# Kernel optimization log

Hardware: AMD Instinct MI355X
Metric: run time of the kernel (lower is better)

Reference implementation:

```python
import jax, jax.numpy as jnp
import numpy as np

H = 1024
W = 1024
SAMPLES_PER_SEG = 32
SIGMA_AA = 1.0
EDGE_CHUNK = 32  # matches torch chunk_size


def sample_bezier_path(control_points):
    # control_points: [N, 2], N = 3*S + 1 cubic segments
    N = control_points.shape[0]
    S = (N - 1) // 3
    idx = 3 * jnp.arange(S)
    p0 = control_points[idx][:, None, :]      # [S,1,2]
    p1 = control_points[idx + 1][:, None, :]
    p2 = control_points[idx + 2][:, None, :]
    p3 = control_points[idx + 3][:, None, :]
    t = jnp.linspace(0.0, 1.0, SAMPLES_PER_SEG, dtype=control_points.dtype)[None, :, None]  # [1,T,1]
    mt = 1.0 - t
    pts = (mt * mt * mt) * p0 + 3.0 * (mt * mt) * t * p1 + 3.0 * mt * (t * t) * p2 + (t * t * t) * p3
    return pts.reshape(S * SAMPLES_PER_SEG, 2)  # [M,2]


def compute_winding(path_points, sigma):
    # path_points: [M,2]; closed polygon edges (j -> (j+1)%M)
    M = path_points.shape[0]
    nxt = jnp.roll(path_points, -1, axis=0)
    x0, y0 = path_points[:, 0], path_points[:, 1]
    x1, y1 = nxt[:, 0], nxt[:, 1]
    dy = y1 - y0
    dx = x1 - x0
    # edges with |dy| < 1e-6 are skipped in the original (continue) -> zero contribution
    coeff = jnp.sign(dy) * (jnp.abs(dy) >= 1e-6).astype(path_points.dtype)
    grid_y = jnp.arange(H, dtype=path_points.dtype)  # rows
    grid_x = jnp.arange(W, dtype=path_points.dtype)  # cols

    n_chunks = M // EDGE_CHUNK
    def chunk_it(a):
        return a.reshape(n_chunks, EDGE_CHUNK)

    def body(acc, c):
        cx0, cy0, cdy, cdx, cc = c  # each [CH]
        t_cross = (grid_y[None, :] - cy0[:, None]) / (cdy[:, None] + 1e-8)          # [CH,H]
        x_cross = cx0[:, None] + t_cross * cdx[:, None]                              # [CH,H]
        valid_t = jax.nn.sigmoid(t_cross * 20.0) * jax.nn.sigmoid((1.0 - t_cross) * 20.0)  # [CH,H]
        crosses = jax.nn.sigmoid((x_cross[:, :, None] - grid_x[None, None, :]) / sigma)    # [CH,H,W]
        contrib = jnp.sum(crosses * (valid_t * cc[:, None])[:, :, None], axis=0)           # [H,W]
        return acc + contrib, None

    init = jnp.zeros((H, W), dtype=path_points.dtype)
    winding, _ = jax.lax.scan(body, init, (chunk_it(x0), chunk_it(y0), chunk_it(dy), chunk_it(dx), chunk_it(coeff)))
    return winding


def setup_inputs() -> dict:
    key = jax.random.key(0)
    k1, k2 = jax.random.split(key)
    control_points = jax.random.uniform(k1, (49, 2), dtype=jnp.float32) * jnp.float32(W)
    color = jax.random.uniform(k2, (3,), dtype=jnp.float32)
    return {"control_points": control_points, "color": color}


def reference(control_points, color):
    pts = sample_bezier_path(control_points)          # [M,2]
    winding = compute_winding(pts, SIGMA_AA)          # [H,W]
    alpha = jax.nn.sigmoid(winding * 4.0)             # [H,W]
    rgb = jnp.broadcast_to(color[None, None, :], (H, W, 3))
    rgba = jnp.concatenate([rgb, alpha[..., None]], axis=-1)  # [H,W,4]
    return rgba
```

## Files before the change

### kernel.cpp

```cpp
#include <hip/hip_runtime.h>

#define HH 1024
#define WW 1024
#define NPTS 512
#define W_EPS 1e-6f

__device__ __forceinline__ float sigmoidf(float z) {
    float e = __expf(-z);
    return __builtin_amdgcn_rcpf(1.0f + e);
}

__global__ __launch_bounds__(256) void render_kernel(
    const float* __restrict__ cp,
    const float* __restrict__ color,
    float* __restrict__ out)
{
    __shared__ float2 pts[NPTS];
    __shared__ float2 act[NPTS];
    __shared__ int n_act;

    const int tid = threadIdx.x;
    const int y = blockIdx.x;
    const float yf = (float)y;

    if (tid == 0) n_act = 0;

    for (int i = tid; i < NPTS; i += 256) {
        int seg = i >> 5;
        int j = i & 31;
        float t = (float)j / 31.0f;
        float mt = 1.0f - t;
        int b = 3 * seg * 2;
        float p0x = cp[b + 0], p0y = cp[b + 1];
        float p1x = cp[b + 2], p1y = cp[b + 3];
        float p2x = cp[b + 4], p2y = cp[b + 5];
        float p3x = cp[b + 6], p3y = cp[b + 7];
        float a0 = mt * mt * mt;
        float a1 = 3.0f * mt * mt * t;
        float a2 = 3.0f * mt * t * t;
        float a3 = t * t * t;
        pts[i] = make_float2(a0 * p0x + a1 * p1x + a2 * p2x + a3 * p3x,
                             a0 * p0y + a1 * p1y + a2 * p2y + a3 * p3y);
    }
    __syncthreads();

    for (int e = tid; e < NPTS; e += 256) {
        float2 p = pts[e];
        float2 q = pts[(e + 1) & (NPTS - 1)];
        float dy = q.y - p.y;
        float dx = q.x - p.x;
        float c = (dy > 0.0f) ? 1.0f : ((dy < 0.0f) ? -1.0f : 0.0f);
        if (fabsf(dy) < 1e-6f) c = 0.0f;
        float t = (yf - p.y) / (dy + 1e-8f);
        float vt = sigmoidf(t * 20.0f) * sigmoidf((1.0f - t) * 20.0f);
        float w = vt * c;
        if (fabsf(w) > W_EPS) {
            float xc = p.x + t * dx;
            int idx = atomicAdd(&n_act, 1);
            act[idx] = make_float2(xc, w);
        }
    }
    __syncthreads();

    const int n = n_act;
    const float r = color[0], g = color[1], b = color[2];

    float acc0 = 0.0f, acc1 = 0.0f, acc2 = 0.0f, acc3 = 0.0f;
    const float x0 = (float)tid;
    const float x1 = (float)(256 + tid);
    const float x2 = (float)(512 + tid);
    const float x3 = (float)(768 + tid);

    for (int e = 0; e < n; ++e) {
        float2 d = act[e];
        acc0 = fmaf(d.y, sigmoidf(d.x - x0), acc0);
        acc1 = fmaf(d.y, sigmoidf(d.x - x1), acc1);
        acc2 = fmaf(d.y, sigmoidf(d.x - x2), acc2);
        acc3 = fmaf(d.y, sigmoidf(d.x - x3), acc3);
    }

    float4* orow = ((float4*)out) + y * WW;
    orow[tid]       = make_float4(r, g, b, sigmoidf(4.0f * acc0));
    orow[256 + tid] = make_float4(r, g, b, sigmoidf(4.0f * acc1));
    orow[512 + tid] = make_float4(r, g, b, sigmoidf(4.0f * acc2));
    orow[768 + tid] = make_float4(r, g, b, sigmoidf(4.0f * acc3));
}

extern "C" void kernel_launch(void* const* d_in, const int* in_sizes, int n_in,
                              void* d_out, int out_size, void* d_ws, size_t ws_size,
                              hipStream_t stream) {
    const float* cp = (const float*)d_in[0];
    const float* color = (const float*)d_in[1];
    float* out = (float*)d_out;
    render_kernel<<<HH, 256, 0, stream>>>(cp, color, out);
}
```

Measured before the change: 67.96 us.

## Bin active edges into 64-pixel tiles and replace saturated sigmoids with constants

Each active edge crossing is assigned to the 64-wide x tiles where its sigmoid is neither saturated to 1 nor to 0. Tiles left of the transition window take the edge weight as a per-tile constant via a prefix sum, and only the edges in a tile's bucket are evaluated per pixel. The aim is to cut the per-pixel sigmoid evaluations from all active edges down to the nearby ones. It adds shared-memory atomics, a fallback path when a bucket overflows, and a small approximation error from treating the saturated tails as exactly 0 or 1.

```diff
diff --git a/kernel.cpp b/kernel.cpp
--- a/kernel.cpp
+++ b/kernel.cpp
@@ -4,6 +4,7 @@
 #define WW 1024
 #define NPTS 512
 #define W_EPS 1e-6f
+#define CAP 64
 
 __device__ __forceinline__ float sigmoidf(float z) {
     float e = __expf(-z);
@@ -16,25 +17,31 @@
     float* __restrict__ out)
 {
     __shared__ float2 pts[NPTS];
-    __shared__ float2 act[NPTS];
-    __shared__ int n_act;
+    __shared__ float2 actXW[NPTS];
+    __shared__ int    actTmin[NPTS];
+    __shared__ int    actTmax[NPTS];
+    __shared__ float2 bucket[16][CAP];
+    __shared__ int    cnt[16];
+    __shared__ float  satW[16];
+    __shared__ int    n_act;
 
     const int tid = threadIdx.x;
     const int y = blockIdx.x;
     const float yf = (float)y;
 
     if (tid == 0) n_act = 0;
+    if (tid < 16) cnt[tid] = 0;
 
     for (int i = tid; i < NPTS; i += 256) {
         int seg = i >> 5;
         int j = i & 31;
         float t = (float)j / 31.0f;
         float mt = 1.0f - t;
-        int b = 3 * seg * 2;
-        float p0x = cp[b + 0], p0y = cp[b + 1];
-        float p1x = cp[b + 2], p1y = cp[b + 3];
-        float p2x = cp[b + 4], p2y = cp[b + 5];
-        float p3x = cp[b + 6], p3y = cp[b + 7];
+        int bb = 3 * seg * 2;
+        float p0x = cp[bb + 0], p0y = cp[bb + 1];
+        float p1x = cp[bb + 2], p1y = cp[bb + 3];
+        float p2x = cp[bb + 4], p2y = cp[bb + 5];
+        float p3x = cp[bb + 6], p3y = cp[bb + 7];
         float a0 = mt * mt * mt;
         float a1 = 3.0f * mt * mt * t;
         float a2 = 3.0f * mt * t * t;
@@ -56,34 +63,70 @@
         float w = vt * c;
         if (fabsf(w) > W_EPS) {
             float xc = p.x + t * dx;
+            int tmin = (int)ceilf((xc - 77.0f) * 0.015625f);
+            if (tmin < 0) tmin = 0;
+            if (tmin > 16) tmin = 16;
+            int tmax = (int)floorf((xc + 14.0f) * 0.015625f);
+            if (tmax > 15) tmax = 15;
             int idx = atomicAdd(&n_act, 1);
-            act[idx] = make_float2(xc, w);
+            actXW[idx] = make_float2(xc, w);
+            actTmin[idx] = tmin;
+            actTmax[idx] = tmax;
+            for (int tt = tmin; tt <= tmax; ++tt) {
+                int pos = atomicAdd(&cnt[tt], 1);
+                if (pos < CAP) bucket[tt][pos] = make_float2(xc, w);
+            }
         }
     }
     __syncthreads();
 
     const int n = n_act;
-    const float r = color[0], g = color[1], b = color[2];
 
-    float acc0 = 0.0f, acc1 = 0.0f, acc2 = 0.0f, acc3 = 0.0f;
-    const float x0 = (float)tid;
-    const float x1 = (float)(256 + tid);
-    const float x2 = (float)(512 + tid);
-    const float x3 = (float)(768 + tid);
+    {
+        int grp = tid >> 4;
+        int l16 = tid & 15;
+        float partial = 0.0f;
+        for (int i = l16; i < n; i += 16)
+            if (grp < actTmin[i]) partial += actXW[i].y;
+        partial += __shfl_down(partial, 8, 16);
+        partial += __shfl_down(partial, 4, 16);
+        partial += __shfl_down(partial, 2, 16);
+        partial += __shfl_down(partial, 1, 16);
+        if (l16 == 0) satW[grp] = partial;
+    }
+    __syncthreads();
 
-    for (int e = 0; e < n; ++e) {
-        float2 d = act[e];
-        acc0 = fmaf(d.y, sigmoidf(d.x - x0), acc0);
-        acc1 = fmaf(d.y, sigmoidf(d.x - x1), acc1);
-        acc2 = fmaf(d.y, sigmoidf(d.x - x2), acc2);
-        acc3 = fmaf(d.y, sigmoidf(d.x - x3), acc3);
+    const float cr = color[0], cg = color[1], cb = color[2];
+    const int wv = tid >> 6;
+    const int lane = tid & 63;
+    float4* orow = ((float4*)out) + y * WW;
+
+    for (int k = 0; k < 4; ++k) {
+        const int t = k * 4 + wv;
+        const int x = t * 64 + lane;
+        const float xf = (float)x;
+        float acc;
+        const int m = cnt[t];
+        if (m <= CAP) {
+            acc = satW[t];
+            for (int j = 0; j < m; ++j) {
+                float2 d = bucket[t][j];
+                acc = fmaf(d.y, sigmoidf(d.x - xf), acc);
+            }
+        } else {
+            acc = 0.0f;
+            for (int i = 0; i < n; ++i) {
+                int tmin = actTmin[i];
+                if (t < tmin) {
+                    acc += actXW[i].y;
+                } else if (t <= actTmax[i]) {
+                    float2 d = actXW[i];
+                    acc = fmaf(d.y, sigmoidf(d.x - xf), acc);
+                }
+            }
+        }
+        orow[x] = make_float4(cr, cg, cb, sigmoidf(4.0f * acc));
     }
-
-    float4* orow = ((float4*)out) + y * WW;
-    orow[tid]       = make_float4(r, g, b, sigmoidf(4.0f * acc0));
-    orow[256 + tid] = make_float4(r, g, b, sigmoidf(4.0f * acc1));
-    orow[512 + tid] = make_float4(r, g, b, sigmoidf(4.0f * acc2));
-    orow[768 + tid] = make_float4(r, g, b, sigmoidf(4.0f * acc3));
 }
 
 extern "C" void kernel_launch(void* const* d_in, const int* in_sizes, int n_in,
```

Result: faster. 64.56 us (-5.0%).

## Bucket active crossings per 64-pixel tile and saturate far-left edges

Applied to the files above, without the earlier changes.

Each block now handles two rows and sorts every active edge crossing into the 64-pixel column tiles where its sigmoid is not saturated. Edges that lie entirely to the right of a tile are folded into a precomputed saturated weight sum, so each pixel evaluates only the nearby crossings instead of all of them. Tiles whose bucket overflows the fixed capacity fall back to a full scan. Saturating the sigmoid to exactly 1 or 0 beyond the chosen margins is an approximation, and it adds shared-memory atomics and extra synchronisation passes.

```diff
diff --git a/kernel.cpp b/kernel.cpp
--- a/kernel.cpp
+++ b/kernel.cpp
@@ -3,87 +3,161 @@
 #define HH 1024
 #define WW 1024
 #define NPTS 512
+#define ROWS 2
+#define TPB 256
 #define W_EPS 1e-6f
+#define CAP 32
 
 __device__ __forceinline__ float sigmoidf(float z) {
     float e = __expf(-z);
     return __builtin_amdgcn_rcpf(1.0f + e);
 }
 
-__global__ __launch_bounds__(256) void render_kernel(
+__global__ __launch_bounds__(TPB) void render_kernel(
     const float* __restrict__ cp,
     const float* __restrict__ color,
     float* __restrict__ out)
 {
+    __shared__ float  cpL[98];
+    __shared__ float  colL[3];
     __shared__ float2 pts[NPTS];
-    __shared__ float2 act[NPTS];
-    __shared__ int n_act;
+    __shared__ float2 actXW[ROWS][NPTS];
+    __shared__ int    actTMM[ROWS][NPTS];
+    __shared__ float2 bucket[ROWS][16][CAP];
+    __shared__ int    cnt[ROWS][16];
+    __shared__ float  satW[ROWS][16];
+    __shared__ int    n_act[ROWS];
 
     const int tid = threadIdx.x;
-    const int y = blockIdx.x;
-    const float yf = (float)y;
+    const int y0 = blockIdx.x * ROWS;
 
-    if (tid == 0) n_act = 0;
+    if (tid < 98) cpL[tid] = cp[tid];
+    if (tid < 3)  colL[tid] = color[tid];
+    if (tid < ROWS) n_act[tid] = 0;
+    if (tid < ROWS * 16) ((int*)cnt)[tid] = 0;
+    {
+        float4* bz = (float4*)bucket;
+        const int NZ = ROWS * 16 * CAP / 2;
+        for (int i = tid; i < NZ; i += TPB) bz[i] = make_float4(0.f, 0.f, 0.f, 0.f);
+    }
+    __syncthreads();
 
-    for (int i = tid; i < NPTS; i += 256) {
+    for (int i = tid; i < NPTS; i += TPB) {
         int seg = i >> 5;
         int j = i & 31;
-        float t = (float)j / 31.0f;
+        float t = (float)j * (1.0f / 31.0f);
         float mt = 1.0f - t;
-        int b = 3 * seg * 2;
-        float p0x = cp[b + 0], p0y = cp[b + 1];
-        float p1x = cp[b + 2], p1y = cp[b + 3];
-        float p2x = cp[b + 4], p2y = cp[b + 5];
-        float p3x = cp[b + 6], p3y = cp[b + 7];
+        int b = 6 * seg;
         float a0 = mt * mt * mt;
         float a1 = 3.0f * mt * mt * t;
         float a2 = 3.0f * mt * t * t;
         float a3 = t * t * t;
-        pts[i] = make_float2(a0 * p0x + a1 * p1x + a2 * p2x + a3 * p3x,
-                             a0 * p0y + a1 * p1y + a2 * p2y + a3 * p3y);
+        pts[i] = make_float2(
+            a0 * cpL[b+0] + a1 * cpL[b+2] + a2 * cpL[b+4] + a3 * cpL[b+6],
+            a0 * cpL[b+1] + a1 * cpL[b+3] + a2 * cpL[b+5] + a3 * cpL[b+7]);
     }
     __syncthreads();
 
-    for (int e = tid; e < NPTS; e += 256) {
+    for (int k = 0; k < ROWS * NPTS / TPB; ++k) {
+        int id = tid + k * TPB;
+        int r = id >> 9;
+        int e = id & (NPTS - 1);
+        float yf = (float)(y0 + r);
         float2 p = pts[e];
         float2 q = pts[(e + 1) & (NPTS - 1)];
         float dy = q.y - p.y;
         float dx = q.x - p.x;
         float c = (dy > 0.0f) ? 1.0f : ((dy < 0.0f) ? -1.0f : 0.0f);
         if (fabsf(dy) < 1e-6f) c = 0.0f;
-        float t = (yf - p.y) / (dy + 1e-8f);
+        float t = (yf - p.y) * __builtin_amdgcn_rcpf(dy + 1e-8f);
         float vt = sigmoidf(t * 20.0f) * sigmoidf((1.0f - t) * 20.0f);
         float w = vt * c;
         if (fabsf(w) > W_EPS) {
-            float xc = p.x + t * dx;
-            int idx = atomicAdd(&n_act, 1);
-            act[idx] = make_float2(xc, w);
+            float xc = fmaf(t, dx, p.x);
+            int tmin = (int)ceilf((xc - 77.0f) * 0.015625f);
+            tmin = max(0, min(16, tmin));
+            int tmax = (int)floorf((xc + 14.0f) * 0.015625f);
+            tmax = max(-1, min(15, tmax));
+            int idx = atomicAdd(&n_act[r], 1);
+            actXW[r][idx] = make_float2(xc, w);
+            actTMM[r][idx] = tmin | ((tmax + 1) << 8);
+            for (int tt = tmin; tt <= tmax; ++tt) {
+                int pos = atomicAdd(&cnt[r][tt], 1);
+                if (pos < CAP) bucket[r][tt][pos] = make_float2(xc, w);
+            }
         }
     }
     __syncthreads();
 
-    const int n = n_act;
-    const float r = color[0], g = color[1], b = color[2];
+    {
+        int pidx = tid >> 3;
+        int sub  = tid & 7;
+        int r = pidx >> 4;
+        int t = pidx & 15;
+        float partial = 0.0f;
+        int n = n_act[r];
+        for (int i = sub; i < n; i += 8) {
+            int tmin = actTMM[r][i] & 0xff;
+            if (t < tmin) partial += actXW[r][i].y;
+        }
+        partial += __shfl_down(partial, 4, 8);
+        partial += __shfl_down(partial, 2, 8);
+        partial += __shfl_down(partial, 1, 8);
+        if (sub == 0) satW[r][t] = partial;
+    }
+    __syncthreads();
 
-    float acc0 = 0.0f, acc1 = 0.0f, acc2 = 0.0f, acc3 = 0.0f;
-    const float x0 = (float)tid;
-    const float x1 = (float)(256 + tid);
-    const float x2 = (float)(512 + tid);
-    const float x3 = (float)(768 + tid);
+    const int wv = tid >> 6;
+    const int lane = tid & 63;
+    const int r = wv >> 1;
+    const int h = wv & 1;
+    const float cr = colL[0], cg = colL[1], cb = colL[2];
+    float4* orow = ((float4*)out) + (y0 + r) * WW;
+    const int n = n_act[r];
 
-    for (int e = 0; e < n; ++e) {
-        float2 d = act[e];
-        acc0 = fmaf(d.y, sigmoidf(d.x - x0), acc0);
-        acc1 = fmaf(d.y, sigmoidf(d.x - x1), acc1);
-        acc2 = fmaf(d.y, sigmoidf(d.x - x2), acc2);
-        acc3 = fmaf(d.y, sigmoidf(d.x - x3), acc3);
+    for (int k = 0; k < 2; ++k) {
+        const int tb = h * 8 + k * 4;
+        float acc0 = satW[r][tb+0], acc1 = satW[r][tb+1];
+        float acc2 = satW[r][tb+2], acc3 = satW[r][tb+3];
+        const int m0 = cnt[r][tb+0], m1 = cnt[r][tb+1];
+        const int m2 = cnt[r][tb+2], m3 = cnt[r][tb+3];
+        int mmax = max(max(min(m0,CAP), min(m1,CAP)), max(min(m2,CAP), min(m3,CAP)));
+        const float xf0 = (float)(tb * 64 + lane);
+
+        for (int j = 0; j < mmax; ++j) {
+            float2 d0 = bucket[r][tb+0][j];
+            float2 d1 = bucket[r][tb+1][j];
+            float2 d2 = bucket[r][tb+2][j];
+            float2 d3 = bucket[r][tb+3][j];
+            acc0 = fmaf(d0.y, sigmoidf(d0.x - xf0),            acc0);
+            acc1 = fmaf(d1.y, sigmoidf(d1.x - (xf0 +  64.0f)), acc1);
+            acc2 = fmaf(d2.y, sigmoidf(d2.x - (xf0 + 128.0f)), acc2);
+            acc3 = fmaf(d3.y, sigmoidf(d3.x - (xf0 + 192.0f)), acc3);
+        }
+
+        float accs[4] = {acc0, acc1, acc2, acc3};
+        const int ms[4] = {m0, m1, m2, m3};
+        for (int c = 0; c < 4; ++c) {
+            const int t = tb + c;
+            if (ms[c] > CAP) {
+                const float xf = (float)(t * 64 + lane);
+                float a = satW[r][t];
+                for (int i = 0; i < n; ++i) {
+                    int tmm = actTMM[r][i];
+                    int tmin = tmm & 0xff;
+                    int tmax = (tmm >> 8) - 1;
+                    if (t < tmin) {
+                        a += actXW[r][i].y;
+                    } else if (t <= tmax) {
+                        float2 d = actXW[r][i];
+                        a = fmaf(d.y, sigmoidf(d.x - xf), a);
+                    }
+                }
+                accs[c] = a;
+            }
+            orow[t * 64 + lane] = make_float4(cr, cg, cb, sigmoidf(4.0f * accs[c]));
+        }
     }
-
-    float4* orow = ((float4*)out) + y * WW;
-    orow[tid]       = make_float4(r, g, b, sigmoidf(4.0f * acc0));
-    orow[256 + tid] = make_float4(r, g, b, sigmoidf(4.0f * acc1));
-    orow[512 + tid] = make_float4(r, g, b, sigmoidf(4.0f * acc2));
-    orow[768 + tid] = make_float4(r, g, b, sigmoidf(4.0f * acc3));
 }
 
 extern "C" void kernel_launch(void* const* d_in, const int* in_sizes, int n_in,
@@ -92,5 +166,5 @@
     const float* cp = (const float*)d_in[0];
     const float* color = (const float*)d_in[1];
     float* out = (float*)d_out;
-    render_kernel<<<HH, 256, 0, stream>>>(cp, color, out);
+    render_kernel<<<HH / ROWS, TPB, 0, stream>>>(cp, color, out);
 }
```

Measured after the change: 66.59 us. 2.0% less time.
